# Kernel optimization log

Hardware: AMD Instinct MI355X
Metric: run time of the kernel (lower is better)

Reference implementation:

```python
import jax, jax.numpy as jnp
import numpy as np

NUM_GRAPHS = 16  # static number of graphs for pooling
BN_EPS = 1e-5


def gat_layer(x, W, a_src, a_dst, src, dst, N, concat):
    # x: (N, Fin), W: (H, Fin, Fout), a_src/a_dst: (H, Fout)
    Wh = jnp.einsum('ni,hio->hno', x, W)                      # (H, N, Fout)
    e_src = jnp.einsum('hno,ho->hn', Wh, a_src)               # (H, N)
    e_dst = jnp.einsum('hno,ho->hn', Wh, a_dst)               # (H, N)
    e = jax.nn.leaky_relu(e_src[:, src] + e_dst[:, dst], 0.2)  # (H, E)
    # edge softmax over incoming edges per dst; torch code starts max at 0
    seg_max = jax.vmap(lambda eh: jax.ops.segment_max(eh, dst, num_segments=N))(e)
    e_max = jnp.maximum(seg_max, 0.0)                         # (H, N)
    exp_e = jnp.exp(e - e_max[:, dst])                        # (H, E)
    exp_sum = jax.vmap(lambda eh: jax.ops.segment_sum(eh, dst, num_segments=N))(exp_e)
    attn = exp_e / (exp_sum[:, dst] + 1e-8)                   # (H, E)
    msgs = attn[:, :, None] * Wh[:, src]                      # (H, E, Fout)
    out = jax.vmap(lambda m: jax.ops.segment_sum(m, dst, num_segments=N))(msgs)  # (H, N, Fout)
    if concat:
        out = jnp.transpose(out, (1, 0, 2)).reshape(N, -1)
    else:
        out = out.mean(axis=0)
    return out, attn


def batchnorm(h, gamma, beta):
    mu = h.mean(axis=0)
    var = h.var(axis=0)
    return (h - mu) / jnp.sqrt(var + BN_EPS) * gamma + beta


def setup_inputs() -> dict:
    key = jax.random.key(0)
    ks = jax.random.split(key, 20)
    N, E = 50000, 400000
    IN, HID, H, NC = 262, 128, 4, 2

    def xavier(k, shape):
        fan_in, fan_out = shape[-2], shape[-1]
        lim = np.sqrt(6.0 / (fan_in + fan_out))
        return jax.random.uniform(k, shape, jnp.float32, -lim, lim)

    x = jax.random.normal(ks[0], (N, IN), jnp.float32)
    edge_index = jax.random.randint(ks[1], (2, E), 0, N, jnp.int64)
    batch = jnp.sort(jax.random.randint(ks[2], (N,), 0, NUM_GRAPHS, jnp.int64))

    return {
        'x': x, 'edge_index': edge_index, 'batch': batch,
        'W1': xavier(ks[3], (H, IN, HID)),
        'a_src1': xavier(ks[4], (H, HID, 1)).squeeze(-1),
        'a_dst1': xavier(ks[5], (H, HID, 1)).squeeze(-1),
        'W2': xavier(ks[6], (1, HID * H, HID)),
        'a_src2': xavier(ks[7], (1, HID, 1)).squeeze(-1),
        'a_dst2': xavier(ks[8], (1, HID, 1)).squeeze(-1),
        'bn1_g': jnp.ones((HID * H,), jnp.float32),
        'bn1_b': jnp.zeros((HID * H,), jnp.float32),
        'bn2_g': jnp.ones((HID,), jnp.float32),
        'bn2_b': jnp.zeros((HID,), jnp.float32),
        'cls_w1': xavier(ks[9], (HID, HID // 2)),
        'cls_b1': jnp.zeros((HID // 2,), jnp.float32),
        'cls_w2': xavier(ks[10], (HID // 2, NC)),
        'cls_b2': jnp.zeros((NC,), jnp.float32),
        'ep_w1': xavier(ks[11], (HID * 2, HID)),
        'ep_b1': jnp.zeros((HID,), jnp.float32),
        'ep_w2': xavier(ks[12], (HID, 1)),
        'ep_b2': jnp.zeros((1,), jnp.float32),
    }


def reference(x, edge_index, batch, W1, a_src1, a_dst1, W2, a_src2, a_dst2,
              bn1_g, bn1_b, bn2_g, bn2_b, cls_w1, cls_b1, cls_w2, cls_b2,
              ep_w1, ep_b1, ep_w2, ep_b2):
    N = x.shape[0]
    src, dst = edge_index[0], edge_index[1]

    h1, _ = gat_layer(x, W1, a_src1, a_dst1, src, dst, N, concat=True)
    h1 = batchnorm(jax.nn.elu(h1), bn1_g, bn1_b)

    h2, attn2 = gat_layer(h1, W2, a_src2, a_dst2, src, dst, N, concat=False)
    h2 = batchnorm(jax.nn.elu(h2), bn2_g, bn2_b)

    # global mean pool over graphs
    sums = jax.ops.segment_sum(h2, batch, num_segments=NUM_GRAPHS)
    counts = jax.ops.segment_sum(jnp.ones((N,), h2.dtype), batch, num_segments=NUM_GRAPHS)
    graph_repr = sums / jnp.clip(counts, 1.0)[:, None]

    logits = jax.nn.relu(graph_repr @ cls_w1 + cls_b1) @ cls_w2 + cls_b2

    edge_feat = jnp.concatenate([h2[src], h2[dst]], axis=1)  # (E, 2*hidden)
    importance = jax.nn.sigmoid(
        (jax.nn.relu(edge_feat @ ep_w1 + ep_b1) @ ep_w2 + ep_b2).squeeze(-1))

    gat_attention = jnp.transpose(attn2, (1, 0))  # (E, 1)
    return logits, h2, importance, gat_attention
```

## Files before the change

### kernel.cpp

```cpp
#include <hip/hip_runtime.h>
#include <hip/hip_bf16.h>
#include <math.h>

typedef __hip_bfloat16 bf16;
typedef __bf16 bf16x8 __attribute__((ext_vector_type(8)));
typedef __bf16 bf16x2v __attribute__((ext_vector_type(2)));
typedef float f32x4 __attribute__((ext_vector_type(4)));

#define NN 50000
#define EE 400000
#define FIN 262
#define KP1 288
#define HID 128
#define NH 4
#define C1 512
#define NGR 16
#define SCAN_NB ((NN + 255) / 256)

__device__ __forceinline__ float b2f(bf16 x){ return __bfloat162float(x); }
__device__ __forceinline__ bf16 f2b(float x){ return __float2bfloat16(x); }
__device__ __forceinline__ float lrelu(float v){ return v >= 0.f ? v : 0.2f * v; }
__device__ __forceinline__ float eluf(float v){ return v > 0.f ? v : expm1f(v); }

__global__ void zero_words(unsigned int* __restrict__ p, int n) {
  int i = blockIdx.x * 256 + threadIdx.x;
  if (i < n) p[i] = 0u;
}

__global__ __launch_bounds__(256)
void gemm_mfma(const bf16* __restrict__ A, const bf16* __restrict__ Bt,
               bf16* __restrict__ C, int M, int K, int Ncols,
               const float* __restrict__ sc, const float* __restrict__ sh) {
  __shared__ __align__(16) __bf16 As[128 * 40];
  __shared__ __align__(16) __bf16 Bs[128 * 40];
  int bm = blockIdx.y * 128, bn = blockIdx.x * 128;
  int tid = threadIdx.x;
  int wave = tid >> 6, lane = tid & 63;
  int quad = lane >> 4, l16 = lane & 15;
  int wm = (wave >> 1) * 64, wn = (wave & 1) * 64;
  f32x4 acc[4][4];
  #pragma unroll
  for (int i = 0; i < 4; ++i)
    #pragma unroll
    for (int j = 0; j < 4; ++j)
      acc[i][j] = (f32x4){0.f, 0.f, 0.f, 0.f};

  for (int k0 = 0; k0 < K; k0 += 32) {
    #pragma unroll
    for (int l = 0; l < 2; ++l) {
      int e = l * 2048 + tid * 8;
      int row = e >> 5, col = e & 31;
      uint4 va = {0u, 0u, 0u, 0u};
      int gm = bm + row;
      if (gm < M) {
        va = *(const uint4*)(A + (size_t)gm * K + k0 + col);
        if (sc) {
          bf16x8 a8 = *(bf16x8*)&va;
          float4 c0 = *(const float4*)(sc + k0 + col);
          float4 c1 = *(const float4*)(sc + k0 + col + 4);
          float4 h0 = *(const float4*)(sh + k0 + col);
          float4 h1v = *(const float4*)(sh + k0 + col + 4);
          bf16x8 t8;
          t8[0] = (__bf16)((float)a8[0] * c0.x + h0.x);
          t8[1] = (__bf16)((float)a8[1] * c0.y + h0.y);
          t8[2] = (__bf16)((float)a8[2] * c0.z + h0.z);
          t8[3] = (__bf16)((float)a8[3] * c0.w + h0.w);
          t8[4] = (__bf16)((float)a8[4] * c1.x + h1v.x);
          t8[5] = (__bf16)((float)a8[5] * c1.y + h1v.y);
          t8[6] = (__bf16)((float)a8[6] * c1.z + h1v.z);
          t8[7] = (__bf16)((float)a8[7] * c1.w + h1v.w);
          va = *(uint4*)&t8;
        }
      }
      *(uint4*)(&As[row * 40 + col]) = va;
      uint4 vb = {0u, 0u, 0u, 0u};
      int gn = bn + row;
      if (gn < Ncols) vb = *(const uint4*)(Bt + (size_t)gn * K + k0 + col);
      *(uint4*)(&Bs[row * 40 + col]) = vb;
    }
    __syncthreads();
    bf16x8 af[4], bf_[4];
    #pragma unroll
    for (int i = 0; i < 4; ++i)
      af[i] = *(const bf16x8*)(&As[(wm + i * 16 + l16) * 40 + quad * 8]);
    #pragma unroll
    for (int j = 0; j < 4; ++j)
      bf_[j] = *(const bf16x8*)(&Bs[(wn + j * 16 + l16) * 40 + quad * 8]);
    #pragma unroll
    for (int i = 0; i < 4; ++i)
      #pragma unroll
      for (int j = 0; j < 4; ++j)
        acc[i][j] = __builtin_amdgcn_mfma_f32_16x16x32_bf16(af[i], bf_[j], acc[i][j], 0, 0, 0);
    __syncthreads();
  }
  #pragma unroll
  for (int i = 0; i < 4; ++i) {
    #pragma unroll
    for (int r = 0; r < 4; ++r) {
      int gm = bm + wm + i * 16 + quad * 4 + r;
      if (gm >= M) continue;
      #pragma unroll
      for (int j = 0; j < 4; ++j) {
        int gn = bn + wn + j * 16 + l16;
        C[(size_t)gm * Ncols + gn] = f2b(acc[i][j][r]);
      }
    }
  }
}

__global__ void conv_x(const float* __restrict__ x, bf16* __restrict__ xb) {
  int i = blockIdx.x * 256 + threadIdx.x;
  if (i >= NN * KP1) return;
  int row = i / KP1, col = i - row * KP1;
  xb[i] = (col < FIN) ? f2b(x[(size_t)row * FIN + col]) : f2b(0.f);
}
__global__ void prep_b1t(const float* __restrict__ W1, bf16* __restrict__ B1t) {
  int i = blockIdx.x * 256 + threadIdx.x;
  if (i >= C1 * KP1) return;
  int n = i / KP1, k = i - n * KP1;
  int h = n >> 7, o = n & 127;
  B1t[i] = (k < FIN) ? f2b(W1[((size_t)h * FIN + k) * HID + o]) : f2b(0.f);
}
__global__ void prep_b2t(const float* __restrict__ W2, bf16* __restrict__ B2t) {
  int i = blockIdx.x * 256 + threadIdx.x;
  if (i >= HID * C1) return;
  int n = i >> 9, k = i & 511;
  B2t[i] = f2b(W2[(size_t)k * HID + n]);
}
__global__ void prep_bpt(const float* __restrict__ epw1, bf16* __restrict__ BPt) {
  int i = blockIdx.x * 256 + threadIdx.x;
  if (i >= 256 * HID) return;
  int n = i >> 7, k = i & 127;
  float v = (n < 128) ? epw1[(size_t)k * HID + n] : epw1[(size_t)(128 + k) * HID + (n - 128)];
  BPt[i] = f2b(v);
}

__global__ void edot_all(const bf16* __restrict__ Wh1, const float* __restrict__ av,
                         const float* __restrict__ bv, float* __restrict__ es1,
                         float* __restrict__ ed1) {
  int wid = threadIdx.x >> 6, lane = threadIdx.x & 63;
  int n = blockIdx.x * 4 + wid;
  if (n >= NN) return;
  int h = lane >> 4, c16 = lane & 15;
  int fbase = h * HID + c16 * 8;
  bf16x8 r = *(const bf16x8*)(Wh1 + (size_t)n * C1 + fbase);
  float s1 = 0.f, s2 = 0.f;
  #pragma unroll
  for (int j = 0; j < 8; ++j) {
    float rv = (float)r[j];
    s1 += rv * av[fbase + j];
    s2 += rv * bv[fbase + j];
  }
  #pragma unroll
  for (int off = 8; off > 0; off >>= 1) {
    s1 += __shfl_xor(s1, off);
    s2 += __shfl_xor(s2, off);
  }
  if (c16 == 0) { es1[n * 4 + h] = s1; ed1[n * 4 + h] = s2; }
}

__global__ void edot1(const bf16* __restrict__ Wh, const float* __restrict__ av,
                      const float* __restrict__ bv, float* __restrict__ es,
                      float* __restrict__ ed) {
  int wid = threadIdx.x >> 6, lane = threadIdx.x & 63;
  int r = blockIdx.x * 4 + wid;
  if (r >= NN) return;
  const bf16* row = Wh + (size_t)r * HID;
  float w0 = b2f(row[lane]), w1 = b2f(row[lane + 64]);
  float s1 = w0 * av[lane] + w1 * av[lane + 64];
  float s2 = w0 * bv[lane] + w1 * bv[lane + 64];
  #pragma unroll
  for (int off = 32; off > 0; off >>= 1) {
    s1 += __shfl_xor(s1, off);
    s2 += __shfl_xor(s2, off);
  }
  if (lane == 0) { es[r] = s1; ed[r] = s2; }
}

__global__ void count_kernel(const int* __restrict__ dst, int* __restrict__ deg, int E) {
  int e = blockIdx.x * blockDim.x + threadIdx.x;
  if (e >= E) return;
  int d = dst[e];
  if ((unsigned)d < NN) atomicAdd(&deg[d], 1);
}

__global__ void scan_p1(const int* __restrict__ deg, int* __restrict__ bsum) {
  __shared__ int s[256];
  int t = threadIdx.x;
  int i = blockIdx.x * 256 + t;
  s[t] = (i < NN) ? deg[i] : 0;
  __syncthreads();
  #pragma unroll
  for (int off = 128; off > 0; off >>= 1) {
    if (t < off) s[t] += s[t + off];
    __syncthreads();
  }
  if (t == 0) bsum[blockIdx.x] = s[0];
}
__global__ void scan_p2(const int* __restrict__ bsum, int* __restrict__ boff,
                        int* __restrict__ total_out) {
  __shared__ int s[256];
  int t = threadIdx.x;
  s[t] = (t < SCAN_NB) ? bsum[t] : 0;
  __syncthreads();
  if (t == 0) {
    int r = 0;
    for (int i = 0; i < SCAN_NB; ++i) { int v = s[i]; s[i] = r; r += v; }
    total_out[0] = r;
  }
  __syncthreads();
  if (t < SCAN_NB) boff[t] = s[t];
}
__global__ void scan_p3(const int* __restrict__ deg, const int* __restrict__ boff,
                        int* __restrict__ rowptr, int* __restrict__ cursor) {
  __shared__ int s[256];
  int t = threadIdx.x;
  int i = blockIdx.x * 256 + t;
  int v = (i < NN) ? deg[i] : 0;
  s[t] = v;
  __syncthreads();
  #pragma unroll
  for (int off = 1; off < 256; off <<= 1) {
    int add = (t >= off) ? s[t - off] : 0;
    __syncthreads();
    s[t] += add;
    __syncthreads();
  }
  if (i < NN) {
    int pos = boff[blockIdx.x] + s[t] - v;
    rowptr[i] = pos;
    cursor[i] = pos;
  }
}

__global__ void scatter_kernel(const int* __restrict__ src, const int* __restrict__ dst,
                               int* __restrict__ cursor, int* __restrict__ csr_s,
                               int* __restrict__ csr_d, int* __restrict__ csr_e, int E) {
  int e = blockIdx.x * blockDim.x + threadIdx.x;
  if (e >= E) return;
  int d = dst[e];
  if ((unsigned)d >= NN) return;
  int s = src[e]; if ((unsigned)s >= NN) s = 0;
  int p = atomicAdd(&cursor[d], 1);
  if ((unsigned)p < (unsigned)E) { csr_s[p] = s; csr_d[p] = d; csr_e[p] = e; }
}

__global__ void logits1(const int* __restrict__ csr_s, const int* __restrict__ csr_d,
                        const float4* __restrict__ es1, const float4* __restrict__ ed1,
                        float4* __restrict__ v1, int* __restrict__ m1i) {
  int j = blockIdx.x * 256 + threadIdx.x;
  if (j >= EE) return;
  int s = csr_s[j]; if ((unsigned)s >= NN) s = 0;
  int d = csr_d[j]; if ((unsigned)d >= NN) d = 0;
  float4 a = es1[s], bb = ed1[d];
  float4 v;
  v.x = lrelu(a.x + bb.x);
  v.y = lrelu(a.y + bb.y);
  v.z = lrelu(a.z + bb.z);
  v.w = lrelu(a.w + bb.w);
  v1[j] = v;
  if (v.x > 0.f) atomicMax(&m1i[d * 4 + 0], __float_as_int(v.x));
  if (v.y > 0.f) atomicMax(&m1i[d * 4 + 1], __float_as_int(v.y));
  if (v.z > 0.f) atomicMax(&m1i[d * 4 + 2], __float_as_int(v.z));
  if (v.w > 0.f) atomicMax(&m1i[d * 4 + 3], __float_as_int(v.w));
}

__global__ void logits2(const int* __restrict__ csr_s, const int* __restrict__ csr_d,
                        const float* __restrict__ es2, const float* __restrict__ ed2,
                        float* __restrict__ v2, int* __restrict__ m2i) {
  int j = blockIdx.x * 256 + threadIdx.x;
  if (j >= EE) return;
  int s = csr_s[j]; if ((unsigned)s >= NN) s = 0;
  int d = csr_d[j]; if ((unsigned)d >= NN) d = 0;
  float v = lrelu(es2[s] + ed2[d]);
  v2[j] = v;
  if (v > 0.f) atomicMax(&m2i[d], __float_as_int(v));
}

__global__ __launch_bounds__(256, 5)
void agg1_all(const int* __restrict__ csr_s, const int* __restrict__ rowptr,
              const float* __restrict__ lg, const float* __restrict__ mx,
              const bf16* __restrict__ Wh1, bf16* __restrict__ h1) {
  int wid = threadIdx.x >> 6, lane = threadIdx.x & 63;
  int node = blockIdx.x * 4 + wid;
  if (node >= NN) return;
  int b = rowptr[node], e = rowptr[node + 1];
  if (b < 0) b = 0; if (e > EE) e = EE;
  int h = lane >> 4;
  float m = mx[node * 4 + h];
  float sum = 0.f;
  float acc[8] = {};
  for (int j = b; j < e; j += 8) {
    int s_[8]; float w[8];
    #pragma unroll
    for (int i = 0; i < 8; ++i) {
      int t = j + i;
      int jj = t < e ? t : (e - 1);
      s_[i] = csr_s[jj];
      w[i] = lg[jj * 4 + h];
    }
    bf16x8 r[8];
    #pragma unroll
    for (int i = 0; i < 8; ++i)
      r[i] = *(const bf16x8*)(Wh1 + (size_t)s_[i] * C1 + lane * 8);
    #pragma unroll
    for (int i = 0; i < 8; ++i) {
      float p = (j + i < e) ? __expf(w[i] - m) : 0.f;
      sum += p;
      #pragma unroll
      for (int k = 0; k < 8; ++k) acc[k] += p * (float)r[i][k];
    }
  }
  float scale = 1.f / (sum + 1e-8f);
  bf16x8 o;
  #pragma unroll
  for (int k = 0; k < 8; ++k) o[k] = (__bf16)eluf(acc[k] * scale);
  *(bf16x8*)(h1 + (size_t)node * C1 + lane * 8) = o;
}

__global__ __launch_bounds__(256, 8)
void agg2_all(const int* __restrict__ csr_s, const int* __restrict__ rowptr,
              const float* __restrict__ lg, const float* __restrict__ mx,
              const bf16* __restrict__ Wh2, bf16* __restrict__ h2p,
              float* __restrict__ invs2) {
  int tid = threadIdx.x;
  int l16 = tid & 15;
  int node = blockIdx.x * 16 + (tid >> 4);
  if (node >= NN) return;
  int b = rowptr[node], e = rowptr[node + 1];
  if (b < 0) b = 0; if (e > EE) e = EE;
  float m = mx[node];
  float sum = 0.f;
  float acc[8] = {};
  for (int j = b; j < e; j += 4) {
    int s_[4]; float w[4];
    #pragma unroll
    for (int i = 0; i < 4; ++i) {
      int t = j + i;
      int jj = t < e ? t : (e - 1);
      s_[i] = csr_s[jj];
      w[i] = lg[jj];
    }
    bf16x8 r[4];
    #pragma unroll
    for (int i = 0; i < 4; ++i)
      r[i] = *(const bf16x8*)(Wh2 + (size_t)s_[i] * HID + l16 * 8);
    #pragma unroll
    for (int i = 0; i < 4; ++i) {
      float p = (j + i < e) ? __expf(w[i] - m) : 0.f;
      sum += p;
      #pragma unroll
      for (int k = 0; k < 8; ++k) acc[k] += p * (float)r[i][k];
    }
  }
  float scale = 1.f / (sum + 1e-8f);
  bf16x8 o;
  #pragma unroll
  for (int k = 0; k < 8; ++k) o[k] = (__bf16)eluf(acc[k] * scale);
  *(bf16x8*)(h2p + (size_t)node * HID + l16 * 8) = o;
  if (l16 == 0) invs2[node] = scale;
}

__global__ void attn_csr(const int* __restrict__ csr_d, const int* __restrict__ csr_e,
                         const float* __restrict__ lg, const float* __restrict__ mx,
                         const float* __restrict__ invs2, float* __restrict__ out) {
  int j = blockIdx.x * 256 + threadIdx.x;
  if (j >= EE) return;
  int d = csr_d[j]; if ((unsigned)d >= NN) d = 0;
  int e = csr_e[j]; if ((unsigned)e >= EE) return;
  out[e] = __expf(lg[j] - mx[d]) * invs2[d];
}

__global__ void stats_ro(const bf16* __restrict__ X, float* __restrict__ cs,
                         float* __restrict__ cq, int Nrows, int C) {
  int c = threadIdx.x;
  int rpb = (Nrows + gridDim.x - 1) / gridDim.x;
  int r0 = blockIdx.x * rpb, r1 = min(r0 + rpb, Nrows);
  float s = 0.f, s2 = 0.f;
  for (int r = r0; r < r1; ++r) {
    float v = b2f(X[(size_t)r * C + c]);
    s += v; s2 += v * v;
  }
  atomicAdd(&cs[c], s);
  atomicAdd(&cq[c], s2);
}

__global__ void bn_coef(const float* __restrict__ cs, const float* __restrict__ cq,
                        const float* __restrict__ gamma, const float* __restrict__ beta,
                        float* __restrict__ sc, float* __restrict__ sh, int C, float invN) {
  int c = blockIdx.x * 256 + threadIdx.x;
  if (c >= C) return;
  float mu = cs[c] * invN;
  float var = cq[c] * invN - mu * mu;
  float g = rsqrtf(fmaxf(var, 0.f) + 1e-5f) * gamma[c];
  sc[c] = g;
  sh[c] = beta[c] - mu * g;
}

__global__ void bn_apply(const bf16* __restrict__ in, bf16* __restrict__ out,
                         float* __restrict__ out2,
                         const float* __restrict__ cs, const float* __restrict__ cq,
                         const float* __restrict__ gamma, const float* __restrict__ beta,
                         int C, size_t total, float invN) {
  size_t i = (size_t)blockIdx.x * blockDim.x + threadIdx.x;
  if (i >= total) return;
  int c = (int)(i % C);
  float mu = cs[c] * invN;
  float var = cq[c] * invN - mu * mu;
  float v = (b2f(in[i]) - mu) * rsqrtf(fmaxf(var, 0.f) + 1e-5f) * gamma[c] + beta[c];
  out[i] = f2b(v);
  if (out2) out2[i] = v;
}

__global__ __launch_bounds__(256)
void pool_kernel(const bf16* __restrict__ h2, const int* __restrict__ batch,
                 float* __restrict__ pooled) {
  int t = threadIdx.x;
  int f = t & 127, half = t >> 7;
  int r0 = blockIdx.x * 32;
  int g_cur = -1;
  float acc = 0.f;
  #pragma unroll
  for (int i = 0; i < 16; ++i) {
    int r = r0 + half + 2 * i;
    if (r >= NN) break;
    int g = batch[r]; if ((unsigned)g >= NGR) g = 0;
    float v = b2f(h2[(size_t)r * HID + f]);
    if (g != g_cur) {
      if (g_cur >= 0) atomicAdd(&pooled[g_cur * HID + f], acc);
      g_cur = g; acc = 0.f;
    }
    acc += v;
  }
  if (g_cur >= 0) atomicAdd(&pooled[g_cur * HID + f], acc);
}

__global__ void cnt_kernel(const int* __restrict__ batch, float* __restrict__ cnt) {
  int g = threadIdx.x;
  if (g >= NGR) return;
  int a = 0, b = NN;
  while (a < b) { int m = (a + b) >> 1; if (batch[m] < g) a = m + 1; else b = m; }
  int lb = a;
  a = 0; b = NN;
  while (a < b) { int m = (a + b) >> 1; if (batch[m] <= g) a = m + 1; else b = m; }
  cnt[g] = (float)(a - lb);
}

__global__ void cls_kernel(const float* __restrict__ pooled, const float* __restrict__ cnt,
                           const float* __restrict__ w1, const float* __restrict__ b1,
                           const float* __restrict__ w2, const float* __restrict__ b2,
                           float* __restrict__ out) {
  __shared__ float repr[NGR * HID];
  __shared__ float hid[NGR * 64];
  int t = threadIdx.x;
  for (int i = t; i < NGR * HID; i += 128) {
    int g = i >> 7;
    repr[i] = pooled[i] / fmaxf(cnt[g], 1.f);
  }
  __syncthreads();
  for (int i = t; i < NGR * 64; i += 128) {
    int g = i >> 6, j = i & 63;
    float s = b1[j];
    for (int c = 0; c < HID; ++c) s += repr[g * HID + c] * w1[c * 64 + j];
    hid[i] = fmaxf(s, 0.f);
  }
  __syncthreads();
  if (t < NGR * 2) {
    int g = t >> 1, k = t & 1;
    float s = b2[k];
    for (int j = 0; j < 64; ++j) s += hid[g * 64 + j] * w2[j * 2 + k];
    out[t] = s;
  }
}

__global__ __launch_bounds__(256)
void eimp_kernel(const int* __restrict__ csr_s, const int* __restrict__ csr_d,
                 const int* __restrict__ csr_e, const bf16* __restrict__ PQ,
                 const float* __restrict__ b1, const float* __restrict__ w2,
                 const float* __restrict__ b2, float* __restrict__ out) {
  int tid = threadIdx.x;
  int wave = tid >> 6, lane = tid & 63;
  int g = lane >> 4, l16 = lane & 15;
  int slot = blockIdx.x * 16 + wave * 4 + g;
  if (slot >= EE) return;
  int s = csr_s[slot]; if ((unsigned)s >= NN) s = 0;
  int d = csr_d[slot]; if ((unsigned)d >= NN) d = 0;
  int e = csr_e[slot]; if ((unsigned)e >= EE) return;
  bf16x8 p = *(const bf16x8*)(PQ + (size_t)s * 256 + l16 * 8);
  bf16x8 q = *(const bf16x8*)(PQ + (size_t)d * 256 + 128 + l16 * 8);
  float acc = 0.f;
  #pragma unroll
  for (int r = 0; r < 8; ++r) {
    int jj = l16 * 8 + r;
    float hh = (float)p[r] + (float)q[r] + b1[jj];
    hh = fmaxf(hh, 0.f);
    acc += hh * w2[jj];
  }
  #pragma unroll
  for (int off = 8; off > 0; off >>= 1) acc += __shfl_xor(acc, off);
  if (l16 == 0) {
    float z = acc + b2[0];
    out[e] = 1.f / (1.f + expf(-z));
  }
}

extern "C" void kernel_launch(void* const* d_in, const int* in_sizes, int n_in,
                              void* d_out, int out_size, void* d_ws, size_t ws_size,
                              hipStream_t stream) {
  const float* x      = (const float*)d_in[0];
  const int*   ei     = (const int*)d_in[1];
  const int*   batch  = (const int*)d_in[2];
  const float* W1     = (const float*)d_in[3];
  const float* a_src1 = (const float*)d_in[4];
  const float* a_dst1 = (const float*)d_in[5];
  const float* W2     = (const float*)d_in[6];
  const float* a_src2 = (const float*)d_in[7];
  const float* a_dst2 = (const float*)d_in[8];
  const float* bn1_g  = (const float*)d_in[9];
  const float* bn1_b  = (const float*)d_in[10];
  const float* bn2_g  = (const float*)d_in[11];
  const float* bn2_b  = (const float*)d_in[12];
  const float* cls_w1 = (const float*)d_in[13];
  const float* cls_b1 = (const float*)d_in[14];
  const float* cls_w2 = (const float*)d_in[15];
  const float* cls_b2 = (const float*)d_in[16];
  const float* ep_w1  = (const float*)d_in[17];
  const float* ep_b1  = (const float*)d_in[18];
  const float* ep_w2  = (const float*)d_in[19];
  const float* ep_b2  = (const float*)d_in[20];

  const int* srcp = ei;
  const int* dstp = ei + EE;

  char* base = (char*)d_ws;
  bf16* xb   = (bf16*)(base);
  bf16* h1   = (bf16*)(base);
  bf16* Wh1  = (bf16*)(base + 51200000);
  bf16* Wh2  = (bf16*)(base + 51200000);
  bf16* h2p  = (bf16*)(base + 64000000);
  bf16* h2   = (bf16*)(base + 76800000);
  bf16* PQ   = (bf16*)(base + 51200000);
  float* es1   = (float*)(base + 102400000);
  float* ed1   = (float*)(base + 103200000);
  float* v2csr = (float*)(base + 102400000);
  int*   m1i   = (int*)(base + 104000000);
  int*   m2i   = (int*)(base + 104800000);
  int*   deg   = (int*)(base + 105000000);
  float* stats = (float*)(base + 105200000);
  float* cs1 = stats,        *cq1 = stats + 512;
  float* cs2 = stats + 1024, *cq2 = stats + 1152;
  float* pooled = stats + 1280;
  float* cnt    = stats + 3328;
  float* sc1   = (float*)(base + 105213376);
  float* sh1   = (float*)(base + 105215424);
  float* es2   = (float*)(base + 105217472);
  float* ed2   = (float*)(base + 105417472);
  float* invs2 = (float*)(base + 105617472);
  int*   cursor= (int*)(base + 105817472);
  int*   rowptr= (int*)(base + 106017472);
  int*   bsum  = (int*)(base + 106217476);
  int*   boff  = bsum + 256;
  int*   csr_s = (int*)(base + 106219524);
  int*   csr_d = (int*)(base + 107819524);
  int*   csr_e = (int*)(base + 109419524);
  float* v1csr = (float*)(base + 111019536);
  bf16*  B1t   = (bf16*)(base + 117419536);
  bf16*  B2t   = (bf16*)(base + 117714448);
  bf16*  BPt   = (bf16*)(base + 117845520);

  float* out        = (float*)d_out;
  float* out_logits = out;
  float* out_h2     = out + 32;
  float* out_imp    = out + 32 + (size_t)NN * HID;
  float* out_attn   = out_imp + EE;

  zero_words<<<(303344 + 255) / 256, 256, 0, stream>>>((unsigned int*)m1i, 303344);

  conv_x<<<(NN * KP1 + 255) / 256, 256, 0, stream>>>(x, xb);
  prep_b1t<<<(C1 * KP1 + 255) / 256, 256, 0, stream>>>(W1, B1t);
  prep_b2t<<<(HID * C1 + 255) / 256, 256, 0, stream>>>(W2, B2t);
  prep_bpt<<<(256 * HID + 255) / 256, 256, 0, stream>>>(ep_w1, BPt);

  count_kernel<<<(EE + 255) / 256, 256, 0, stream>>>(dstp, deg, EE);
  scan_p1<<<SCAN_NB, 256, 0, stream>>>(deg, bsum);
  scan_p2<<<1, 256, 0, stream>>>(bsum, boff, rowptr + NN);
  scan_p3<<<SCAN_NB, 256, 0, stream>>>(deg, boff, rowptr, cursor);
  scatter_kernel<<<(EE + 255) / 256, 256, 0, stream>>>(srcp, dstp, cursor,
                                                       csr_s, csr_d, csr_e, EE);

  dim3 g1(C1 / 128, (NN + 127) / 128);
  gemm_mfma<<<g1, 256, 0, stream>>>(xb, B1t, Wh1, NN, KP1, C1, nullptr, nullptr);
  edot_all<<<(NN + 3) / 4, 256, 0, stream>>>(Wh1, a_src1, a_dst1, es1, ed1);
  logits1<<<(EE + 255) / 256, 256, 0, stream>>>(csr_s, csr_d, (const float4*)es1,
                                                (const float4*)ed1, (float4*)v1csr, m1i);
  agg1_all<<<(NN + 3) / 4, 256, 0, stream>>>(csr_s, rowptr, v1csr,
                                             (const float*)m1i, Wh1, h1);

  stats_ro<<<400, C1, 0, stream>>>(h1, cs1, cq1, NN, C1);
  bn_coef<<<2, 256, 0, stream>>>(cs1, cq1, bn1_g, bn1_b, sc1, sh1, C1, 1.f / NN);

  dim3 g2(1, (NN + 127) / 128);
  gemm_mfma<<<g2, 256, 0, stream>>>(h1, B2t, Wh2, NN, C1, HID, sc1, sh1);
  edot1<<<(NN + 3) / 4, 256, 0, stream>>>(Wh2, a_src2, a_dst2, es2, ed2);
  logits2<<<(EE + 255) / 256, 256, 0, stream>>>(csr_s, csr_d, es2, ed2, v2csr, m2i);
  agg2_all<<<(NN + 15) / 16, 256, 0, stream>>>(csr_s, rowptr, v2csr,
                                               (const float*)m2i, Wh2, h2p, invs2);
  attn_csr<<<(EE + 255) / 256, 256, 0, stream>>>(csr_d, csr_e, v2csr,
                                                 (const float*)m2i, invs2, out_attn);

  stats_ro<<<400, HID, 0, stream>>>(h2p, cs2, cq2, NN, HID);
  {
    size_t total = (size_t)NN * HID;
    bn_apply<<<(unsigned)((total + 255) / 256), 256, 0, stream>>>(
        h2p, h2, out_h2, cs2, cq2, bn2_g, bn2_b, HID, total, 1.f / NN);
  }

  pool_kernel<<<(NN + 31) / 32, 256, 0, stream>>>(h2, batch, pooled);
  cnt_kernel<<<1, 64, 0, stream>>>(batch, cnt);
  cls_kernel<<<1, 128, 0, stream>>>(pooled, cnt, cls_w1, cls_b1, cls_w2, cls_b2, out_logits);

  dim3 gpq(2, (NN + 127) / 128);
  gemm_mfma<<<gpq, 256, 0, stream>>>(h2, BPt, PQ, NN, HID, 256, nullptr, nullptr);
  eimp_kernel<<<(EE + 15) / 16, 256, 0, stream>>>(csr_s, csr_d, csr_e, PQ,
                                                  ep_b1, ep_w2, ep_b2, out_imp);
}
```

Measured before the change: 638.3 us.

## Fold BN2 affine into pooling, classifier and edge GEMM; peel aggregation tails

The second batchnorm no longer writes a normalized bf16 copy of h2. Pooling runs on the pre-BN activations and the per-channel affine is applied to the pooled means in the classifier. The edge-predictor GEMM reads pre-BN h2 with scale/shift applied in its prologue, and the fp32 output is written by a vectorized bn_out kernel. The aggregation kernels split full 8/4-edge chunks from a remainder loop to remove per-edge bounds selects, and agg1 occupancy hint rises to 6. This saves one bf16 write and read of h2, at the cost of relying on BN being affine so it commutes with mean pooling.

```diff
diff --git a/kernel.cpp b/kernel.cpp
--- a/kernel.cpp
+++ b/kernel.cpp
@@ -277,7 +277,7 @@
   if (v > 0.f) atomicMax(&m2i[d], __float_as_int(v));
 }
 
-__global__ __launch_bounds__(256, 5)
+__global__ __launch_bounds__(256, 6)
 void agg1_all(const int* __restrict__ csr_s, const int* __restrict__ rowptr,
               const float* __restrict__ lg, const float* __restrict__ mx,
               const bf16* __restrict__ Wh1, bf16* __restrict__ h1) {
@@ -290,26 +290,48 @@
   float m = mx[node * 4 + h];
   float sum = 0.f;
   float acc[8] = {};
-  for (int j = b; j < e; j += 8) {
+  const bf16* W = Wh1 + lane * 8;
+  int j = b;
+  for (; j + 8 <= e; j += 8) {
     int s_[8]; float w[8];
     #pragma unroll
+    for (int i = 0; i < 8; ++i) { s_[i] = csr_s[j + i]; w[i] = lg[(j + i) * 4 + h]; }
+    bf16x8 r[8];
+    #pragma unroll
+    for (int i = 0; i < 8; ++i)
+      r[i] = *(const bf16x8*)(W + (size_t)s_[i] * C1);
+    #pragma unroll
     for (int i = 0; i < 8; ++i) {
-      int t = j + i;
-      int jj = t < e ? t : (e - 1);
-      s_[i] = csr_s[jj];
-      w[i] = lg[jj * 4 + h];
-    }
-    bf16x8 r[8];
-    #pragma unroll
-    for (int i = 0; i < 8; ++i)
-      r[i] = *(const bf16x8*)(Wh1 + (size_t)s_[i] * C1 + lane * 8);
-    #pragma unroll
-    for (int i = 0; i < 8; ++i) {
-      float p = (j + i < e) ? __expf(w[i] - m) : 0.f;
+      float p = __expf(w[i] - m);
       sum += p;
       #pragma unroll
       for (int k = 0; k < 8; ++k) acc[k] += p * (float)r[i][k];
     }
+  }
+  if (j + 4 <= e) {
+    int s_[4]; float w[4];
+    #pragma unroll
+    for (int i = 0; i < 4; ++i) { s_[i] = csr_s[j + i]; w[i] = lg[(j + i) * 4 + h]; }
+    bf16x8 r[4];
+    #pragma unroll
+    for (int i = 0; i < 4; ++i)
+      r[i] = *(const bf16x8*)(W + (size_t)s_[i] * C1);
+    #pragma unroll
+    for (int i = 0; i < 4; ++i) {
+      float p = __expf(w[i] - m);
+      sum += p;
+      #pragma unroll
+      for (int k = 0; k < 8; ++k) acc[k] += p * (float)r[i][k];
+    }
+    j += 4;
+  }
+  for (; j < e; ++j) {
+    int s0 = csr_s[j];
+    float p = __expf(lg[j * 4 + h] - m);
+    bf16x8 r0 = *(const bf16x8*)(W + (size_t)s0 * C1);
+    sum += p;
+    #pragma unroll
+    for (int k = 0; k < 8; ++k) acc[k] += p * (float)r0[k];
   }
   float scale = 1.f / (sum + 1e-8f);
   bf16x8 o;
@@ -332,26 +354,31 @@
   float m = mx[node];
   float sum = 0.f;
   float acc[8] = {};
-  for (int j = b; j < e; j += 4) {
+  const bf16* W = Wh2 + l16 * 8;
+  int j = b;
+  for (; j + 4 <= e; j += 4) {
     int s_[4]; float w[4];
     #pragma unroll
+    for (int i = 0; i < 4; ++i) { s_[i] = csr_s[j + i]; w[i] = lg[j + i]; }
+    bf16x8 r[4];
+    #pragma unroll
+    for (int i = 0; i < 4; ++i)
+      r[i] = *(const bf16x8*)(W + (size_t)s_[i] * HID);
+    #pragma unroll
     for (int i = 0; i < 4; ++i) {
-      int t = j + i;
-      int jj = t < e ? t : (e - 1);
-      s_[i] = csr_s[jj];
-      w[i] = lg[jj];
-    }
-    bf16x8 r[4];
-    #pragma unroll
-    for (int i = 0; i < 4; ++i)
-      r[i] = *(const bf16x8*)(Wh2 + (size_t)s_[i] * HID + l16 * 8);
-    #pragma unroll
-    for (int i = 0; i < 4; ++i) {
-      float p = (j + i < e) ? __expf(w[i] - m) : 0.f;
+      float p = __expf(w[i] - m);
       sum += p;
       #pragma unroll
       for (int k = 0; k < 8; ++k) acc[k] += p * (float)r[i][k];
     }
+  }
+  for (; j < e; ++j) {
+    int s0 = csr_s[j];
+    float p = __expf(lg[j] - m);
+    bf16x8 r0 = *(const bf16x8*)(W + (size_t)s0 * HID);
+    sum += p;
+    #pragma unroll
+    for (int k = 0; k < 8; ++k) acc[k] += p * (float)r0[k];
   }
   float scale = 1.f / (sum + 1e-8f);
   bf16x8 o;
@@ -397,19 +424,17 @@
   sh[c] = beta[c] - mu * g;
 }
 
-__global__ void bn_apply(const bf16* __restrict__ in, bf16* __restrict__ out,
-                         float* __restrict__ out2,
-                         const float* __restrict__ cs, const float* __restrict__ cq,
-                         const float* __restrict__ gamma, const float* __restrict__ beta,
-                         int C, size_t total, float invN) {
-  size_t i = (size_t)blockIdx.x * blockDim.x + threadIdx.x;
-  if (i >= total) return;
-  int c = (int)(i % C);
-  float mu = cs[c] * invN;
-  float var = cq[c] * invN - mu * mu;
-  float v = (b2f(in[i]) - mu) * rsqrtf(fmaxf(var, 0.f) + 1e-5f) * gamma[c] + beta[c];
-  out[i] = f2b(v);
-  if (out2) out2[i] = v;
+__global__ void bn_out(const bf16* __restrict__ in, float* __restrict__ out2,
+                       const float* __restrict__ sc, const float* __restrict__ sh) {
+  int i = blockIdx.x * 256 + threadIdx.x;
+  if (i >= NN * HID / 8) return;
+  int c8 = (i & 15) * 8;
+  bf16x8 v = *(const bf16x8*)(in + (size_t)i * 8);
+  float o[8];
+  #pragma unroll
+  for (int k = 0; k < 8; ++k) o[k] = (float)v[k] * sc[c8 + k] + sh[c8 + k];
+  *(float4*)(out2 + (size_t)i * 8)     = make_float4(o[0], o[1], o[2], o[3]);
+  *(float4*)(out2 + (size_t)i * 8 + 4) = make_float4(o[4], o[5], o[6], o[7]);
 }
 
 __global__ __launch_bounds__(256)
@@ -447,6 +472,7 @@
 }
 
 __global__ void cls_kernel(const float* __restrict__ pooled, const float* __restrict__ cnt,
+                           const float* __restrict__ sc2, const float* __restrict__ sh2,
                            const float* __restrict__ w1, const float* __restrict__ b1,
                            const float* __restrict__ w2, const float* __restrict__ b2,
                            float* __restrict__ out) {
@@ -454,8 +480,9 @@
   __shared__ float hid[NGR * 64];
   int t = threadIdx.x;
   for (int i = t; i < NGR * HID; i += 128) {
-    int g = i >> 7;
-    repr[i] = pooled[i] / fmaxf(cnt[g], 1.f);
+    int g = i >> 7, c = i & 127;
+    float c_ = cnt[g];
+    repr[i] = (c_ > 0.f) ? (pooled[i] / c_ * sc2[c] + sh2[c]) : 0.f;
   }
   __syncthreads();
   for (int i = t; i < NGR * 64; i += 128) {
@@ -537,9 +564,8 @@
   bf16* h1   = (bf16*)(base);
   bf16* Wh1  = (bf16*)(base + 51200000);
   bf16* Wh2  = (bf16*)(base + 51200000);
-  bf16* h2p  = (bf16*)(base + 64000000);
-  bf16* h2   = (bf16*)(base + 76800000);
   bf16* PQ   = (bf16*)(base + 51200000);
+  bf16* h2p  = (bf16*)(base + 76800000);
   float* es1   = (float*)(base + 102400000);
   float* ed1   = (float*)(base + 103200000);
   float* v2csr = (float*)(base + 102400000);
@@ -553,20 +579,22 @@
   float* cnt    = stats + 3328;
   float* sc1   = (float*)(base + 105213376);
   float* sh1   = (float*)(base + 105215424);
-  float* es2   = (float*)(base + 105217472);
-  float* ed2   = (float*)(base + 105417472);
-  float* invs2 = (float*)(base + 105617472);
-  int*   cursor= (int*)(base + 105817472);
-  int*   rowptr= (int*)(base + 106017472);
-  int*   bsum  = (int*)(base + 106217476);
+  float* sc2   = (float*)(base + 105217472);
+  float* sh2   = (float*)(base + 105217984);
+  float* es2   = (float*)(base + 105218496);
+  float* ed2   = (float*)(base + 105418496);
+  float* invs2 = (float*)(base + 105618496);
+  int*   cursor= (int*)(base + 105818496);
+  int*   rowptr= (int*)(base + 106018496);
+  int*   bsum  = (int*)(base + 106218560);
   int*   boff  = bsum + 256;
-  int*   csr_s = (int*)(base + 106219524);
-  int*   csr_d = (int*)(base + 107819524);
-  int*   csr_e = (int*)(base + 109419524);
-  float* v1csr = (float*)(base + 111019536);
-  bf16*  B1t   = (bf16*)(base + 117419536);
-  bf16*  B2t   = (bf16*)(base + 117714448);
-  bf16*  BPt   = (bf16*)(base + 117845520);
+  int*   csr_s = (int*)(base + 106220608);
+  int*   csr_d = (int*)(base + 107820608);
+  int*   csr_e = (int*)(base + 109420608);
+  float* v1csr = (float*)(base + 111020608);
+  bf16*  B1t   = (bf16*)(base + 117420608);
+  bf16*  B2t   = (bf16*)(base + 117715520);
+  bf16*  BPt   = (bf16*)(base + 117846592);
 
   float* out        = (float*)d_out;
   float* out_logits = out;
@@ -608,19 +636,18 @@
   attn_csr<<<(EE + 255) / 256, 256, 0, stream>>>(csr_d, csr_e, v2csr,
                                                  (const float*)m2i, invs2, out_attn);
 
+  pool_kernel<<<(NN + 31) / 32, 256, 0, stream>>>(h2p, batch, pooled);
+  cnt_kernel<<<1, 64, 0, stream>>>(batch, cnt);
+
   stats_ro<<<400, HID, 0, stream>>>(h2p, cs2, cq2, NN, HID);
-  {
-    size_t total = (size_t)NN * HID;
-    bn_apply<<<(unsigned)((total + 255) / 256), 256, 0, stream>>>(
-        h2p, h2, out_h2, cs2, cq2, bn2_g, bn2_b, HID, total, 1.f / NN);
-  }
-
-  pool_kernel<<<(NN + 31) / 32, 256, 0, stream>>>(h2, batch, pooled);
-  cnt_kernel<<<1, 64, 0, stream>>>(batch, cnt);
-  cls_kernel<<<1, 128, 0, stream>>>(pooled, cnt, cls_w1, cls_b1, cls_w2, cls_b2, out_logits);
+  bn_coef<<<1, 256, 0, stream>>>(cs2, cq2, bn2_g, bn2_b, sc2, sh2, HID, 1.f / NN);
+  bn_out<<<(NN * HID / 8 + 255) / 256, 256, 0, stream>>>(h2p, out_h2, sc2, sh2);
+
+  cls_kernel<<<1, 128, 0, stream>>>(pooled, cnt, sc2, sh2,
+                                    cls_w1, cls_b1, cls_w2, cls_b2, out_logits);
 
   dim3 gpq(2, (NN + 127) / 128);
-  gemm_mfma<<<gpq, 256, 0, stream>>>(h2, BPt, PQ, NN, HID, 256, nullptr, nullptr);
+  gemm_mfma<<<gpq, 256, 0, stream>>>(h2p, BPt, PQ, NN, HID, 256, sc2, sh2);
   eimp_kernel<<<(EE + 15) / 16, 256, 0, stream>>>(csr_s, csr_d, csr_e, PQ,
                                                   ep_b1, ep_w2, ep_b2, out_imp);
 }
```

Result: no change. 631.5 us (-1.1%).
